# Kernel tuning notes

Measured on AMD Instinct MI355X. Metric: run time of the kernel, lower is better.

## Reference

```python
import jax, jax.numpy as jnp
import numpy as np
import math

B = 524288
D = 4
CTX = 64
HID = 128
IN_DIM = 2 + CTX  # keep_idx len is 2 for every mask
# default_masks_D(4, 10) dedups to exactly these 4 masks (torch module therefore has 4 layers)
KEEP = ((0, 1), (1, 2), (2, 3), (0, 3))
TRANS = ((2, 3), (0, 3), (0, 1), (1, 2))
L = 4


def _mlp(x, W1, b1, W2, b2, W3, b3):
    # MLP(in_dim, out_dim, hidden=128, depth=2): Lin+GELU, Lin+GELU, Lin
    x = jax.nn.gelu(x @ W1 + b1, approximate=False)
    x = jax.nn.gelu(x @ W2 + b2, approximate=False)
    return x @ W3 + b3


def setup_inputs() -> dict:
    key = jax.random.key(0)
    ks = jax.random.split(key, 16)
    theta = jax.random.normal(ks[0], (B, D), dtype=jnp.float32)
    h = jax.random.normal(ks[1], (B, CTX), dtype=jnp.float32)
    p = lambda k, shape: jax.random.normal(k, shape, dtype=jnp.float32) * 0.02
    inp = {"theta": theta, "h": h}
    # stacked per-layer weights for s_net and t_net
    for pref, off in (("s", 2), ("t", 8)):
        inp[pref + "W1"] = p(ks[off + 0], (L, IN_DIM, HID))
        inp[pref + "b1"] = p(ks[off + 1], (L, HID))
        inp[pref + "W2"] = p(ks[off + 2], (L, HID, HID))
        inp[pref + "b2"] = p(ks[off + 3], (L, HID))
        inp[pref + "W3"] = p(ks[off + 4], (L, HID, 2))
        inp[pref + "b3"] = p(ks[off + 5], (L, 2))
    return inp


def reference(theta, h, sW1, sb1, sW2, sb2, sW3, sb3, tW1, tb1, tW2, tb2, tW3, tb3):
    # ConditionalRealNVP.log_prob(theta, h)
    x = theta
    logdet = jnp.zeros(theta.shape[0], dtype=theta.dtype)
    for i in range(L):
        keep = np.array(KEEP[i])
        trans = np.array(TRANS[i])
        xp = jnp.concatenate([x[:, keep], h], axis=1)  # [B, 66]
        s = _mlp(xp, sW1[i], sb1[i], sW2[i], sb2[i], sW3[i], sb3[i])  # [B, 2]
        t = _mlp(xp, tW1[i], tb1[i], tW2[i], tb2[i], tW3[i], tb3[i])  # [B, 2]
        x = x.at[:, trans].set(x[:, trans] * jnp.exp(s) + t)
        logdet = logdet + s.sum(axis=1)
    log_pz = -0.5 * (x ** 2).sum(axis=1) - 0.5 * D * math.log(2 * math.pi)
    return log_pz + logdet
```

## Files before the change

### kernel.cpp

```cpp
#include <hip/hip_runtime.h>
#include <hip/hip_bf16.h>

typedef short short8 __attribute__((ext_vector_type(8)));
typedef float f32x4 __attribute__((ext_vector_type(4)));
typedef float f32x2 __attribute__((ext_vector_type(2)));
typedef unsigned short u16;
typedef unsigned int u32;
typedef u32 u32x4 __attribute__((ext_vector_type(4)));

#define NL_STRIDE 57344
#define OFF_W1F 0
#define OFF_W2F 16384
#define OFF_W3F 49152
#define OFF_W1K 53248
#define OFF_B1  54272
#define OFF_B2  54784
#define OFF_B3  55296

__device__ __forceinline__ u16 f2bf(float f) {
  union { float f; unsigned int u; } v; v.f = f;
  unsigned int r = v.u + 0x7fffu + ((v.u >> 16) & 1u);
  return (u16)(r >> 16);
}

__device__ __forceinline__ u32 pack_bf16_2(float a, float b) {
  union { float f; u32 u; } x, y; x.f = a; y.f = b;
  u32 ra = x.u + 0x8000u, rb = y.u + 0x8000u;
  return (ra >> 16) | (rb & 0xffff0000u);
}

__device__ __forceinline__ f32x2 gelu2(f32x2 x) {
  f32x2 u = x * x;
  f32x2 t = u * 0.00417617f + (-0.0560330f);
  t = t * u + 0.394326f;
  f32x2 s = x * t + 0.5f;
  s.x = __builtin_amdgcn_fmed3f(s.x, 0.0f, 1.0f);
  s.y = __builtin_amdgcn_fmed3f(s.y, 0.0f, 1.0f);
  return x * s;
}

__device__ __forceinline__ int kperm(int k) {
  int b = k & 31;
  return (k & ~31) | ((b >> 1) | ((b & 1) << 4));
}

__global__ __launch_bounds__(256) void prep_kernel(
    const float* __restrict__ sW1, const float* __restrict__ sb1,
    const float* __restrict__ sW2, const float* __restrict__ sb2,
    const float* __restrict__ sW3, const float* __restrict__ sb3,
    const float* __restrict__ tW1, const float* __restrict__ tb1,
    const float* __restrict__ tW2, const float* __restrict__ tb2,
    const float* __restrict__ tW3, const float* __restrict__ tb3,
    char* __restrict__ ws)
{
  int nl = blockIdx.x;
  int layer = nl >> 1, net = nl & 1;
  const float* W1 = net ? tW1 : sW1;
  const float* W2 = net ? tW2 : sW2;
  const float* W3 = net ? tW3 : sW3;
  const float* B1 = net ? tb1 : sb1;
  const float* B2 = net ? tb2 : sb2;
  const float* B3 = net ? tb3 : sb3;
  char* base = ws + (size_t)nl * NL_STRIDE;
  int e = blockIdx.y * 256 + (int)threadIdx.x;

  if (e < 8192) {
    int kt = e >> 12, rem = e & 4095, nt = rem >> 9, r2 = rem & 511;
    int l = r2 >> 3, j = r2 & 7;
    int k = kt * 32 + (l >> 4) * 8 + j, n = nt * 16 + (l & 15);
    ((u16*)(base + OFF_W1F))[e] = f2bf(W1[layer * 8448 + (2 + k) * 128 + n]);
  } else if (e < 24576) {
    int e2 = e - 8192;
    int kt = e2 >> 12, nt = (e2 >> 9) & 7, l = (e2 >> 3) & 63, j = e2 & 7;
    int k = kt * 32 + (l >> 4) * 8 + j, n = nt * 16 + (l & 15);
    ((u16*)(base + OFF_W2F))[e2] = f2bf(W2[layer * 16384 + kperm(k) * 128 + n]);
  } else if (e < 26624) {
    int e3 = e - 24576;
    int kt = e3 >> 9, l = (e3 >> 3) & 63, j = e3 & 7;
    int k = kt * 32 + (l >> 4) * 8 + j, n = l & 15;
    float v = (n < 2) ? W3[layer * 256 + kperm(k) * 2 + n] : 0.0f;
    ((u16*)(base + OFF_W3F))[e3] = f2bf(v);
  } else if (e < 26880) {
    int e4 = e - 26624; int r = e4 >> 7, n = e4 & 127;
    ((float*)(base + OFF_W1K))[e4] = W1[layer * 8448 + r * 128 + n];
  } else if (e < 27008) {
    int e5 = e - 26880; ((float*)(base + OFF_B1))[e5] = B1[layer * 128 + e5];
  } else if (e < 27136) {
    int e6 = e - 27008; ((float*)(base + OFF_B2))[e6] = B2[layer * 128 + e6];
  } else if (e < 27138) {
    int e7 = e - 27136; ((float*)(base + OFF_B3))[e7] = B3[layer * 2 + e7];
  }
}

__global__ __launch_bounds__(256, 2) void realnvp_kernel(
    const float* __restrict__ theta, const float* __restrict__ h_g,
    const char* __restrict__ ws, float* __restrict__ out)
{
  __shared__ __align__(16) u16 hs[128 * 72];
  __shared__ __align__(16) u16 hid[128 * 136];
  __shared__ float x_lds[128 * 4];
  __shared__ float sbuf[2 * 128 * 2];

  const int tid = (int)threadIdx.x;
  const int row0 = (int)blockIdx.x * 128;
  const int wv = tid >> 6, lane = tid & 63, q = lane >> 4, lr = lane & 15;

  if (tid < 128) {
    float4 t4 = *(const float4*)(theta + (size_t)(row0 + tid) * 4);
    x_lds[tid * 4 + 0] = t4.x; x_lds[tid * 4 + 1] = t4.y;
    x_lds[tid * 4 + 2] = t4.z; x_lds[tid * 4 + 3] = t4.w;
  }
  {
    int r = tid >> 1, hf = tid & 1;
    const float* src = h_g + (size_t)(row0 + r) * 64 + hf * 32;
    u16* dst = &hs[r * 72 + hf * 32];
#pragma unroll
    for (int c = 0; c < 32; c += 8) {
      float4 f0 = *(const float4*)(src + c);
      float4 f1 = *(const float4*)(src + c + 4);
      u32x4 o;
      o[0] = pack_bf16_2(f0.x, f0.y);
      o[1] = pack_bf16_2(f0.z, f0.w);
      o[2] = pack_bf16_2(f1.x, f1.y);
      o[3] = pack_bf16_2(f1.z, f1.w);
      *(u32x4*)(dst + c) = o;
    }
  }
  __syncthreads();

  float logdet = 0.0f;
  const f32x4 zero4 = {0.f, 0.f, 0.f, 0.f};
  const int col0 = wv * 32 + lr;
  u32* hidw = (u32*)&hid[wv * 32 + lr * 2];

#pragma unroll 1
  for (int layer = 0; layer < 4; ++layer) {
    int k0 = (0x0210 >> (layer * 4)) & 15;
    int k1 = (0x3321 >> (layer * 4)) & 15;

#pragma unroll 1
    for (int net = 0; net < 2; ++net) {
      const char* base = ws + (size_t)(layer * 2 + net) * NL_STRIDE;
      const u16* w1f = (const u16*)(base + OFF_W1F);
      const u16* w2f = (const u16*)(base + OFF_W2F);
      const u16* w3f = (const u16*)(base + OFF_W3F);
      const float* w1k = (const float*)(base + OFF_W1K);
      const float* b1 = (const float*)(base + OFF_B1);
      const float* b2 = (const float*)(base + OFF_B2);
      const float* b3 = (const float*)(base + OFF_B3);

      f32x4 acc[8][2];
#pragma unroll
      for (int mt = 0; mt < 8; ++mt) { acc[mt][0] = zero4; acc[mt][1] = zero4; }
      {
        const u16* abase = &hs[lr * 72 + q * 8];
#pragma unroll
        for (int kt = 0; kt < 2; ++kt) {
          short8 a[8];
#pragma unroll
          for (int mt = 0; mt < 8; ++mt)
            a[mt] = *(const short8*)(abase + mt * (16 * 72) + kt * 32);
          short8 b0 = *(const short8*)(w1f + (kt * 8 + wv * 2 + 0) * 512 + lane * 8);
          short8 b1v = *(const short8*)(w1f + (kt * 8 + wv * 2 + 1) * 512 + lane * 8);
#pragma unroll
          for (int mt = 0; mt < 8; ++mt) {
            acc[mt][0] = __builtin_amdgcn_mfma_f32_16x16x32_bf16(a[mt], b0, acc[mt][0], 0, 0, 0);
            acc[mt][1] = __builtin_amdgcn_mfma_f32_16x16x32_bf16(a[mt], b1v, acc[mt][1], 0, 0, 0);
          }
        }
      }
      f32x2 wk0 = {w1k[col0],       w1k[col0 + 16]};
      f32x2 wk1 = {w1k[128 + col0], w1k[128 + col0 + 16]};
      f32x2 bb  = {b1[col0],        b1[col0 + 16]};
      __syncthreads();
#pragma unroll
      for (int mt = 0; mt < 8; ++mt) {
        int rb = mt * 16 + q * 4;
#pragma unroll
        for (int r = 0; r < 4; ++r) {
          int row = rb + r;
          float xk0 = x_lds[row * 4 + k0], xk1 = x_lds[row * 4 + k1];
          f32x2 v = {acc[mt][0][r], acc[mt][1][r]};
          v = wk0 * xk0 + v;
          v = wk1 * xk1 + v;
          v = v + bb;
          f32x2 g = gelu2(v);
          hidw[row * 68] = pack_bf16_2(g.x, g.y);
        }
      }
      __syncthreads();

      f32x4 acc2[8][2];
#pragma unroll
      for (int mt = 0; mt < 8; ++mt) { acc2[mt][0] = zero4; acc2[mt][1] = zero4; }
      {
        const u16* hbase = &hid[lr * 136 + q * 8];
#pragma unroll
        for (int kt = 0; kt < 4; ++kt) {
          short8 a[8];
#pragma unroll
          for (int mt = 0; mt < 8; ++mt)
            a[mt] = *(const short8*)(hbase + mt * (16 * 136) + kt * 32);
          short8 b0 = *(const short8*)(w2f + (kt * 8 + wv * 2 + 0) * 512 + lane * 8);
          short8 b1v = *(const short8*)(w2f + (kt * 8 + wv * 2 + 1) * 512 + lane * 8);
#pragma unroll
          for (int mt = 0; mt < 8; ++mt) {
            acc2[mt][0] = __builtin_amdgcn_mfma_f32_16x16x32_bf16(a[mt], b0, acc2[mt][0], 0, 0, 0);
            acc2[mt][1] = __builtin_amdgcn_mfma_f32_16x16x32_bf16(a[mt], b1v, acc2[mt][1], 0, 0, 0);
          }
        }
      }
      f32x2 cb = {b2[col0], b2[col0 + 16]};
      __syncthreads();
#pragma unroll
      for (int mt = 0; mt < 8; ++mt) {
        int rb = mt * 16 + q * 4;
#pragma unroll
        for (int r = 0; r < 4; ++r) {
          int row = rb + r;
          f32x2 v = {acc2[mt][0][r], acc2[mt][1][r]};
          f32x2 g = gelu2(v + cb);
          hidw[row * 68] = pack_bf16_2(g.x, g.y);
        }
      }
      __syncthreads();

      f32x4 acc3[2]; acc3[0] = zero4; acc3[1] = zero4;
#pragma unroll
      for (int kt = 0; kt < 4; ++kt) {
        short8 b = *(const short8*)(w3f + kt * 512 + lane * 8);
#pragma unroll
        for (int i = 0; i < 2; ++i) {
          short8 a = *(const short8*)(&hid[((wv * 2 + i) * 16 + lr) * 136 + kt * 32 + q * 8]);
          acc3[i] = __builtin_amdgcn_mfma_f32_16x16x32_bf16(a, b, acc3[i], 0, 0, 0);
        }
      }
      if (lr < 2) {
        float bbs = b3[lr];
#pragma unroll
        for (int i = 0; i < 2; ++i) {
          int rb = (wv * 2 + i) * 16 + q * 4;
#pragma unroll
          for (int r = 0; r < 4; ++r)
            sbuf[net * 256 + (rb + r) * 2 + lr] = acc3[i][r] + bbs;
        }
      }
      __syncthreads();
    }

    if (tid < 128) {
      float s0 = sbuf[tid * 2 + 0], s1 = sbuf[tid * 2 + 1];
      float t0 = sbuf[256 + tid * 2 + 0], t1 = sbuf[256 + tid * 2 + 1];
      int a0 = (0x1002 >> (layer * 4)) & 15;
      int a1 = (0x2133 >> (layer * 4)) & 15;
      x_lds[tid * 4 + a0] = x_lds[tid * 4 + a0] * __expf(s0) + t0;
      x_lds[tid * 4 + a1] = x_lds[tid * 4 + a1] * __expf(s1) + t1;
      logdet += s0 + s1;
    }
    __syncthreads();
  }

  if (tid < 128) {
    float x0 = x_lds[tid * 4 + 0], x1 = x_lds[tid * 4 + 1];
    float x2 = x_lds[tid * 4 + 2], x3 = x_lds[tid * 4 + 3];
    out[row0 + tid] = -0.5f * (x0 * x0 + x1 * x1 + x2 * x2 + x3 * x3)
                      - 3.6757541328f + logdet;
  }
}

extern "C" void kernel_launch(void* const* d_in, const int* in_sizes, int n_in,
                              void* d_out, int out_size, void* d_ws, size_t ws_size,
                              hipStream_t stream) {
  (void)in_sizes; (void)n_in; (void)out_size; (void)ws_size;
  const float* theta = (const float*)d_in[0];
  const float* h     = (const float*)d_in[1];
  const float* sW1 = (const float*)d_in[2],  *sb1 = (const float*)d_in[3];
  const float* sW2 = (const float*)d_in[4],  *sb2 = (const float*)d_in[5];
  const float* sW3 = (const float*)d_in[6],  *sb3 = (const float*)d_in[7];
  const float* tW1 = (const float*)d_in[8],  *tb1 = (const float*)d_in[9];
  const float* tW2 = (const float*)d_in[10], *tb2 = (const float*)d_in[11];
  const float* tW3 = (const float*)d_in[12], *tb3 = (const float*)d_in[13];
  float* out = (float*)d_out;
  char* ws = (char*)d_ws;

  dim3 pgrid(8, 107);
  prep_kernel<<<pgrid, 256, 0, stream>>>(sW1, sb1, sW2, sb2, sW3, sb3,
                                         tW1, tb1, tW2, tb2, tW3, tb3, ws);
  realnvp_kernel<<<4096, 256, 0, stream>>>(theta, h, (const char*)ws, out);
}
```

Before: 638.6 us.

## Split GEMM work by rows per wave and keep bf16 context in registers

Each wave now owns 32 rows and computes all 128 hidden columns, instead of 32 columns across all 128 rows. The context tile is converted to bf16 once and held in registers as MFMA A-fragments, which removes the shared-memory staging buffer. Bias and first-layer key weights are permuted so they can be read as paired vectors, and the layer loop is fully unrolled with constant indices. Occupancy is raised to 4 blocks per CU. The trade-off is more global/L2 weight loads per wave (B fragments now cover all 8 column tiles) and higher register pressure under the tighter launch bound.

```diff
diff --git a/kernel.cpp b/kernel.cpp
--- a/kernel.cpp
+++ b/kernel.cpp
@@ -82,23 +82,22 @@
     ((u16*)(base + OFF_W3F))[e3] = f2bf(v);
   } else if (e < 26880) {
     int e4 = e - 26624; int r = e4 >> 7, n = e4 & 127;
-    ((float*)(base + OFF_W1K))[e4] = W1[layer * 8448 + r * 128 + n];
+    ((float*)(base + OFF_W1K))[e4] = W1[layer * 8448 + r * 128 + kperm(n)];
   } else if (e < 27008) {
-    int e5 = e - 26880; ((float*)(base + OFF_B1))[e5] = B1[layer * 128 + e5];
+    int e5 = e - 26880; ((float*)(base + OFF_B1))[e5] = B1[layer * 128 + kperm(e5)];
   } else if (e < 27136) {
-    int e6 = e - 27008; ((float*)(base + OFF_B2))[e6] = B2[layer * 128 + e6];
+    int e6 = e - 27008; ((float*)(base + OFF_B2))[e6] = B2[layer * 128 + kperm(e6)];
   } else if (e < 27138) {
     int e7 = e - 27136; ((float*)(base + OFF_B3))[e7] = B3[layer * 2 + e7];
   }
 }
 
-__global__ __launch_bounds__(256, 2) void realnvp_kernel(
+__global__ __launch_bounds__(256, 4) void realnvp_kernel(
     const float* __restrict__ theta, const float* __restrict__ h_g,
     const char* __restrict__ ws, float* __restrict__ out)
 {
-  __shared__ __align__(16) u16 hs[128 * 72];
   __shared__ __align__(16) u16 hid[128 * 136];
-  __shared__ float x_lds[128 * 4];
+  __shared__ __align__(16) float x_lds[128 * 4];
   __shared__ float sbuf[2 * 128 * 2];
 
   const int tid = (int)threadIdx.x;
@@ -110,33 +109,32 @@
     x_lds[tid * 4 + 0] = t4.x; x_lds[tid * 4 + 1] = t4.y;
     x_lds[tid * 4 + 2] = t4.z; x_lds[tid * 4 + 3] = t4.w;
   }
-  {
-    int r = tid >> 1, hf = tid & 1;
-    const float* src = h_g + (size_t)(row0 + r) * 64 + hf * 32;
-    u16* dst = &hs[r * 72 + hf * 32];
-#pragma unroll
-    for (int c = 0; c < 32; c += 8) {
-      float4 f0 = *(const float4*)(src + c);
-      float4 f1 = *(const float4*)(src + c + 4);
-      u32x4 o;
-      o[0] = pack_bf16_2(f0.x, f0.y);
-      o[1] = pack_bf16_2(f0.z, f0.w);
-      o[2] = pack_bf16_2(f1.x, f1.y);
-      o[3] = pack_bf16_2(f1.z, f1.w);
-      *(u32x4*)(dst + c) = o;
+
+  short8 hf[2][2];
+#pragma unroll
+  for (int i = 0; i < 2; ++i)
+#pragma unroll
+    for (int kt = 0; kt < 2; ++kt) {
+      const float* src = h_g + (size_t)(row0 + wv * 32 + i * 16 + lr) * 64 + kt * 32 + q * 8;
+      float4 f0 = *(const float4*)(src);
+      float4 f1 = *(const float4*)(src + 4);
+      union { u32x4 u; short8 s; } cv;
+      cv.u[0] = pack_bf16_2(f0.x, f0.y);
+      cv.u[1] = pack_bf16_2(f0.z, f0.w);
+      cv.u[2] = pack_bf16_2(f1.x, f1.y);
+      cv.u[3] = pack_bf16_2(f1.z, f1.w);
+      hf[i][kt] = cv.s;
     }
-  }
   __syncthreads();
 
   float logdet = 0.0f;
   const f32x4 zero4 = {0.f, 0.f, 0.f, 0.f};
-  const int col0 = wv * 32 + lr;
-  u32* hidw = (u32*)&hid[wv * 32 + lr * 2];
-
-#pragma unroll 1
+  constexpr int KEEP0[4] = {0, 1, 2, 0}, KEEP1[4] = {1, 2, 3, 3};
+  constexpr int TR0[4]   = {2, 0, 0, 1}, TR1[4]   = {3, 3, 1, 2};
+
+#pragma unroll
   for (int layer = 0; layer < 4; ++layer) {
-    int k0 = (0x0210 >> (layer * 4)) & 15;
-    int k1 = (0x3321 >> (layer * 4)) & 15;
+    const int k0 = KEEP0[layer], k1 = KEEP1[layer];
 
 #pragma unroll 1
     for (int net = 0; net < 2; ++net) {
@@ -149,80 +147,87 @@
       const float* b2 = (const float*)(base + OFF_B2);
       const float* b3 = (const float*)(base + OFF_B3);
 
-      f32x4 acc[8][2];
-#pragma unroll
-      for (int mt = 0; mt < 8; ++mt) { acc[mt][0] = zero4; acc[mt][1] = zero4; }
-      {
-        const u16* abase = &hs[lr * 72 + q * 8];
-#pragma unroll
-        for (int kt = 0; kt < 2; ++kt) {
-          short8 a[8];
-#pragma unroll
-          for (int mt = 0; mt < 8; ++mt)
-            a[mt] = *(const short8*)(abase + mt * (16 * 72) + kt * 32);
-          short8 b0 = *(const short8*)(w1f + (kt * 8 + wv * 2 + 0) * 512 + lane * 8);
-          short8 b1v = *(const short8*)(w1f + (kt * 8 + wv * 2 + 1) * 512 + lane * 8);
-#pragma unroll
-          for (int mt = 0; mt < 8; ++mt) {
-            acc[mt][0] = __builtin_amdgcn_mfma_f32_16x16x32_bf16(a[mt], b0, acc[mt][0], 0, 0, 0);
-            acc[mt][1] = __builtin_amdgcn_mfma_f32_16x16x32_bf16(a[mt], b1v, acc[mt][1], 0, 0, 0);
+      f32x4 acc[2][8];
+#pragma unroll
+      for (int i = 0; i < 2; ++i)
+#pragma unroll
+        for (int nt = 0; nt < 8; ++nt) acc[i][nt] = zero4;
+#pragma unroll
+      for (int kt = 0; kt < 2; ++kt)
+#pragma unroll
+        for (int a = 0; a < 4; ++a) {
+          short8 b0 = *(const short8*)(w1f + (kt * 8 + 2 * a + 0) * 512 + lane * 8);
+          short8 b1v = *(const short8*)(w1f + (kt * 8 + 2 * a + 1) * 512 + lane * 8);
+#pragma unroll
+          for (int i = 0; i < 2; ++i) {
+            acc[i][2 * a]     = __builtin_amdgcn_mfma_f32_16x16x32_bf16(hf[i][kt], b0, acc[i][2 * a], 0, 0, 0);
+            acc[i][2 * a + 1] = __builtin_amdgcn_mfma_f32_16x16x32_bf16(hf[i][kt], b1v, acc[i][2 * a + 1], 0, 0, 0);
           }
         }
-      }
-      f32x2 wk0 = {w1k[col0],       w1k[col0 + 16]};
-      f32x2 wk1 = {w1k[128 + col0], w1k[128 + col0 + 16]};
-      f32x2 bb  = {b1[col0],        b1[col0 + 16]};
-      __syncthreads();
-#pragma unroll
-      for (int mt = 0; mt < 8; ++mt) {
-        int rb = mt * 16 + q * 4;
+      f32x2 wk0v[4], wk1v[4], bbv[4];
+#pragma unroll
+      for (int a = 0; a < 4; ++a) {
+        wk0v[a] = *(const f32x2*)(w1k + a * 32 + 2 * lr);
+        wk1v[a] = *(const f32x2*)(w1k + 128 + a * 32 + 2 * lr);
+        bbv[a]  = *(const f32x2*)(b1 + a * 32 + 2 * lr);
+      }
+      __syncthreads();
+#pragma unroll
+      for (int i = 0; i < 2; ++i)
 #pragma unroll
         for (int r = 0; r < 4; ++r) {
-          int row = rb + r;
-          float xk0 = x_lds[row * 4 + k0], xk1 = x_lds[row * 4 + k1];
-          f32x2 v = {acc[mt][0][r], acc[mt][1][r]};
-          v = wk0 * xk0 + v;
-          v = wk1 * xk1 + v;
-          v = v + bb;
-          f32x2 g = gelu2(v);
-          hidw[row * 68] = pack_bf16_2(g.x, g.y);
-        }
-      }
-      __syncthreads();
-
-      f32x4 acc2[8][2];
-#pragma unroll
-      for (int mt = 0; mt < 8; ++mt) { acc2[mt][0] = zero4; acc2[mt][1] = zero4; }
-      {
-        const u16* hbase = &hid[lr * 136 + q * 8];
-#pragma unroll
-        for (int kt = 0; kt < 4; ++kt) {
-          short8 a[8];
-#pragma unroll
-          for (int mt = 0; mt < 8; ++mt)
-            a[mt] = *(const short8*)(hbase + mt * (16 * 136) + kt * 32);
-          short8 b0 = *(const short8*)(w2f + (kt * 8 + wv * 2 + 0) * 512 + lane * 8);
-          short8 b1v = *(const short8*)(w2f + (kt * 8 + wv * 2 + 1) * 512 + lane * 8);
-#pragma unroll
-          for (int mt = 0; mt < 8; ++mt) {
-            acc2[mt][0] = __builtin_amdgcn_mfma_f32_16x16x32_bf16(a[mt], b0, acc2[mt][0], 0, 0, 0);
-            acc2[mt][1] = __builtin_amdgcn_mfma_f32_16x16x32_bf16(a[mt], b1v, acc2[mt][1], 0, 0, 0);
+          int row = wv * 32 + i * 16 + q * 4 + r;
+          f32x4 xr = *(const f32x4*)(x_lds + row * 4);
+          float xk0 = xr[k0], xk1 = xr[k1];
+          u32* wrow = (u32*)&hid[row * 136];
+#pragma unroll
+          for (int a = 0; a < 4; ++a) {
+            f32x2 v = {acc[i][2 * a][r], acc[i][2 * a + 1][r]};
+            v = wk0v[a] * xk0 + v;
+            v = wk1v[a] * xk1 + v;
+            v = v + bbv[a];
+            f32x2 g = gelu2(v);
+            wrow[a * 16 + lr] = pack_bf16_2(g.x, g.y);
           }
         }
-      }
-      f32x2 cb = {b2[col0], b2[col0 + 16]};
-      __syncthreads();
-#pragma unroll
-      for (int mt = 0; mt < 8; ++mt) {
-        int rb = mt * 16 + q * 4;
+      __syncthreads();
+
+      f32x4 acc2[2][8];
+#pragma unroll
+      for (int i = 0; i < 2; ++i)
+#pragma unroll
+        for (int nt = 0; nt < 8; ++nt) acc2[i][nt] = zero4;
+#pragma unroll
+      for (int kt = 0; kt < 4; ++kt) {
+        short8 a0 = *(const short8*)(&hid[(wv * 32 + lr) * 136 + kt * 32 + q * 8]);
+        short8 a1 = *(const short8*)(&hid[(wv * 32 + 16 + lr) * 136 + kt * 32 + q * 8]);
+#pragma unroll
+        for (int a = 0; a < 4; ++a) {
+          short8 b0 = *(const short8*)(w2f + (kt * 8 + 2 * a + 0) * 512 + lane * 8);
+          short8 b1v = *(const short8*)(w2f + (kt * 8 + 2 * a + 1) * 512 + lane * 8);
+          acc2[0][2 * a]     = __builtin_amdgcn_mfma_f32_16x16x32_bf16(a0, b0, acc2[0][2 * a], 0, 0, 0);
+          acc2[1][2 * a]     = __builtin_amdgcn_mfma_f32_16x16x32_bf16(a1, b0, acc2[1][2 * a], 0, 0, 0);
+          acc2[0][2 * a + 1] = __builtin_amdgcn_mfma_f32_16x16x32_bf16(a0, b1v, acc2[0][2 * a + 1], 0, 0, 0);
+          acc2[1][2 * a + 1] = __builtin_amdgcn_mfma_f32_16x16x32_bf16(a1, b1v, acc2[1][2 * a + 1], 0, 0, 0);
+        }
+      }
+      f32x2 cbv[4];
+#pragma unroll
+      for (int a = 0; a < 4; ++a) cbv[a] = *(const f32x2*)(b2 + a * 32 + 2 * lr);
+      __syncthreads();
+#pragma unroll
+      for (int i = 0; i < 2; ++i)
 #pragma unroll
         for (int r = 0; r < 4; ++r) {
-          int row = rb + r;
-          f32x2 v = {acc2[mt][0][r], acc2[mt][1][r]};
-          f32x2 g = gelu2(v + cb);
-          hidw[row * 68] = pack_bf16_2(g.x, g.y);
-        }
-      }
+          int row = wv * 32 + i * 16 + q * 4 + r;
+          u32* wrow = (u32*)&hid[row * 136];
+#pragma unroll
+          for (int a = 0; a < 4; ++a) {
+            f32x2 v = {acc2[i][2 * a][r], acc2[i][2 * a + 1][r]};
+            f32x2 g = gelu2(v + cbv[a]);
+            wrow[a * 16 + lr] = pack_bf16_2(g.x, g.y);
+          }
+        }
       __syncthreads();
 
       f32x4 acc3[2]; acc3[0] = zero4; acc3[1] = zero4;
@@ -251,8 +256,7 @@
     if (tid < 128) {
       float s0 = sbuf[tid * 2 + 0], s1 = sbuf[tid * 2 + 1];
       float t0 = sbuf[256 + tid * 2 + 0], t1 = sbuf[256 + tid * 2 + 1];
-      int a0 = (0x1002 >> (layer * 4)) & 15;
-      int a1 = (0x2133 >> (layer * 4)) & 15;
+      const int a0 = TR0[layer], a1 = TR1[layer];
       x_lds[tid * 4 + a0] = x_lds[tid * 4 + a0] * __expf(s0) + t0;
       x_lds[tid * 4 + a1] = x_lds[tid * 4 + a1] * __expf(s1) + t1;
       logdet += s0 + s1;
```

Result: slower. 802.8 us (+25.7%).

## Split each 128-row block across 8 waves with 2D M/N wave tiling

Applied to the files above, without the earlier changes.

Raises the block from 256 to 512 threads and splits the work across waves in both directions: each wave now handles half the rows (64) and a quarter of the hidden columns. This halves per-wave accumulators and A-fragment registers, which should allow more waves in flight, and W2 B-fragments are now prefetched one k-step ahead. Hidden columns are permuted so each lane writes an adjacent bf16 pair, and the prep kernel permutes W1k, b1 and b2 to match. The cost is redundant B-fragment loads, since both row-halves fetch the same weights, plus more waves taking part in each barrier.

```diff
diff --git a/kernel.cpp b/kernel.cpp
--- a/kernel.cpp
+++ b/kernel.cpp
@@ -82,28 +82,29 @@
     ((u16*)(base + OFF_W3F))[e3] = f2bf(v);
   } else if (e < 26880) {
     int e4 = e - 26624; int r = e4 >> 7, n = e4 & 127;
-    ((float*)(base + OFF_W1K))[e4] = W1[layer * 8448 + r * 128 + n];
+    ((float*)(base + OFF_W1K))[e4] = W1[layer * 8448 + r * 128 + kperm(n)];
   } else if (e < 27008) {
-    int e5 = e - 26880; ((float*)(base + OFF_B1))[e5] = B1[layer * 128 + e5];
+    int e5 = e - 26880; ((float*)(base + OFF_B1))[e5] = B1[layer * 128 + kperm(e5)];
   } else if (e < 27136) {
-    int e6 = e - 27008; ((float*)(base + OFF_B2))[e6] = B2[layer * 128 + e6];
+    int e6 = e - 27008; ((float*)(base + OFF_B2))[e6] = B2[layer * 128 + kperm(e6)];
   } else if (e < 27138) {
     int e7 = e - 27136; ((float*)(base + OFF_B3))[e7] = B3[layer * 2 + e7];
   }
 }
 
-__global__ __launch_bounds__(256, 2) void realnvp_kernel(
+__global__ __launch_bounds__(512, 4) void realnvp_kernel(
     const float* __restrict__ theta, const float* __restrict__ h_g,
     const char* __restrict__ ws, float* __restrict__ out)
 {
   __shared__ __align__(16) u16 hs[128 * 72];
   __shared__ __align__(16) u16 hid[128 * 136];
-  __shared__ float x_lds[128 * 4];
+  __shared__ __align__(16) float x_lds[128 * 4];
   __shared__ float sbuf[2 * 128 * 2];
 
   const int tid = (int)threadIdx.x;
   const int row0 = (int)blockIdx.x * 128;
-  const int wv = tid >> 6, lane = tid & 63, q = lane >> 4, lr = lane & 15;
+  const int wave = tid >> 6, lane = tid & 63, q = lane >> 4, lr = lane & 15;
+  const int mh = wave & 1, nq = wave >> 1;
 
   if (tid < 128) {
     float4 t4 = *(const float4*)(theta + (size_t)(row0 + tid) * 4);
@@ -111,11 +112,11 @@
     x_lds[tid * 4 + 2] = t4.z; x_lds[tid * 4 + 3] = t4.w;
   }
   {
-    int r = tid >> 1, hf = tid & 1;
-    const float* src = h_g + (size_t)(row0 + r) * 64 + hf * 32;
-    u16* dst = &hs[r * 72 + hf * 32];
-#pragma unroll
-    for (int c = 0; c < 32; c += 8) {
+    int r = tid >> 2, sg = tid & 3;
+    const float* src = h_g + (size_t)(row0 + r) * 64 + sg * 16;
+    u16* dst = &hs[r * 72 + sg * 16];
+#pragma unroll
+    for (int c = 0; c < 16; c += 8) {
       float4 f0 = *(const float4*)(src + c);
       float4 f1 = *(const float4*)(src + c + 4);
       u32x4 o;
@@ -130,13 +131,11 @@
 
   float logdet = 0.0f;
   const f32x4 zero4 = {0.f, 0.f, 0.f, 0.f};
-  const int col0 = wv * 32 + lr;
-  u32* hidw = (u32*)&hid[wv * 32 + lr * 2];
 
 #pragma unroll 1
   for (int layer = 0; layer < 4; ++layer) {
-    int k0 = (0x0210 >> (layer * 4)) & 15;
-    int k1 = (0x3321 >> (layer * 4)) & 15;
+    const int k0 = (0x0210 >> (layer * 4)) & 15;
+    const int k1 = (0x3321 >> (layer * 4)) & 15;
 
 #pragma unroll 1
     for (int net = 0; net < 2; ++net) {
@@ -149,101 +148,110 @@
       const float* b2 = (const float*)(base + OFF_B2);
       const float* b3 = (const float*)(base + OFF_B3);
 
-      f32x4 acc[8][2];
-#pragma unroll
-      for (int mt = 0; mt < 8; ++mt) { acc[mt][0] = zero4; acc[mt][1] = zero4; }
+      f32x4 acc[4][2];
+#pragma unroll
+      for (int i = 0; i < 4; ++i) { acc[i][0] = zero4; acc[i][1] = zero4; }
       {
-        const u16* abase = &hs[lr * 72 + q * 8];
+        short8 b00 = *(const short8*)(w1f + (0 * 8 + 2 * nq + 0) * 512 + lane * 8);
+        short8 b01 = *(const short8*)(w1f + (0 * 8 + 2 * nq + 1) * 512 + lane * 8);
+        short8 b10 = *(const short8*)(w1f + (1 * 8 + 2 * nq + 0) * 512 + lane * 8);
+        short8 b11 = *(const short8*)(w1f + (1 * 8 + 2 * nq + 1) * 512 + lane * 8);
+        const u16* abase = &hs[(64 * mh + lr) * 72 + q * 8];
 #pragma unroll
         for (int kt = 0; kt < 2; ++kt) {
-          short8 a[8];
-#pragma unroll
-          for (int mt = 0; mt < 8; ++mt)
-            a[mt] = *(const short8*)(abase + mt * (16 * 72) + kt * 32);
-          short8 b0 = *(const short8*)(w1f + (kt * 8 + wv * 2 + 0) * 512 + lane * 8);
-          short8 b1v = *(const short8*)(w1f + (kt * 8 + wv * 2 + 1) * 512 + lane * 8);
-#pragma unroll
-          for (int mt = 0; mt < 8; ++mt) {
-            acc[mt][0] = __builtin_amdgcn_mfma_f32_16x16x32_bf16(a[mt], b0, acc[mt][0], 0, 0, 0);
-            acc[mt][1] = __builtin_amdgcn_mfma_f32_16x16x32_bf16(a[mt], b1v, acc[mt][1], 0, 0, 0);
-          }
-        }
-      }
-      f32x2 wk0 = {w1k[col0],       w1k[col0 + 16]};
-      f32x2 wk1 = {w1k[128 + col0], w1k[128 + col0 + 16]};
-      f32x2 bb  = {b1[col0],        b1[col0 + 16]};
-      __syncthreads();
-#pragma unroll
-      for (int mt = 0; mt < 8; ++mt) {
-        int rb = mt * 16 + q * 4;
+          short8 A0 = *(const short8*)(abase + 0 * (16 * 72) + kt * 32);
+          short8 A1 = *(const short8*)(abase + 1 * (16 * 72) + kt * 32);
+          short8 A2 = *(const short8*)(abase + 2 * (16 * 72) + kt * 32);
+          short8 A3 = *(const short8*)(abase + 3 * (16 * 72) + kt * 32);
+          short8 b0 = kt ? b10 : b00, b1v = kt ? b11 : b01;
+          acc[0][0] = __builtin_amdgcn_mfma_f32_16x16x32_bf16(A0, b0, acc[0][0], 0, 0, 0);
+          acc[1][0] = __builtin_amdgcn_mfma_f32_16x16x32_bf16(A1, b0, acc[1][0], 0, 0, 0);
+          acc[2][0] = __builtin_amdgcn_mfma_f32_16x16x32_bf16(A2, b0, acc[2][0], 0, 0, 0);
+          acc[3][0] = __builtin_amdgcn_mfma_f32_16x16x32_bf16(A3, b0, acc[3][0], 0, 0, 0);
+          acc[0][1] = __builtin_amdgcn_mfma_f32_16x16x32_bf16(A0, b1v, acc[0][1], 0, 0, 0);
+          acc[1][1] = __builtin_amdgcn_mfma_f32_16x16x32_bf16(A1, b1v, acc[1][1], 0, 0, 0);
+          acc[2][1] = __builtin_amdgcn_mfma_f32_16x16x32_bf16(A2, b1v, acc[2][1], 0, 0, 0);
+          acc[3][1] = __builtin_amdgcn_mfma_f32_16x16x32_bf16(A3, b1v, acc[3][1], 0, 0, 0);
+        }
+      }
+      f32x2 wk0 = *(const f32x2*)(w1k + nq * 32 + 2 * lr);
+      f32x2 wk1 = *(const f32x2*)(w1k + 128 + nq * 32 + 2 * lr);
+      f32x2 bb  = *(const f32x2*)(b1 + nq * 32 + 2 * lr);
+#pragma unroll
+      for (int i = 0; i < 4; ++i)
 #pragma unroll
         for (int r = 0; r < 4; ++r) {
-          int row = rb + r;
+          int row = 64 * mh + 16 * i + q * 4 + r;
           float xk0 = x_lds[row * 4 + k0], xk1 = x_lds[row * 4 + k1];
-          f32x2 v = {acc[mt][0][r], acc[mt][1][r]};
+          f32x2 v = {acc[i][0][r], acc[i][1][r]};
           v = wk0 * xk0 + v;
           v = wk1 * xk1 + v;
           v = v + bb;
           f32x2 g = gelu2(v);
-          hidw[row * 68] = pack_bf16_2(g.x, g.y);
-        }
-      }
-      __syncthreads();
-
-      f32x4 acc2[8][2];
-#pragma unroll
-      for (int mt = 0; mt < 8; ++mt) { acc2[mt][0] = zero4; acc2[mt][1] = zero4; }
+          ((u32*)&hid[row * 136])[nq * 16 + lr] = pack_bf16_2(g.x, g.y);
+        }
+      __syncthreads();
+
+      f32x4 acc2[4][2];
+#pragma unroll
+      for (int i = 0; i < 4; ++i) { acc2[i][0] = zero4; acc2[i][1] = zero4; }
       {
-        const u16* hbase = &hid[lr * 136 + q * 8];
+        const u16* hbase = &hid[(64 * mh + lr) * 136 + q * 8];
+        short8 nb0 = *(const short8*)(w2f + (0 * 8 + 2 * nq + 0) * 512 + lane * 8);
+        short8 nb1 = *(const short8*)(w2f + (0 * 8 + 2 * nq + 1) * 512 + lane * 8);
+        short8 pb0 = *(const short8*)(w2f + (1 * 8 + 2 * nq + 0) * 512 + lane * 8);
+        short8 pb1 = *(const short8*)(w2f + (1 * 8 + 2 * nq + 1) * 512 + lane * 8);
 #pragma unroll
         for (int kt = 0; kt < 4; ++kt) {
-          short8 a[8];
-#pragma unroll
-          for (int mt = 0; mt < 8; ++mt)
-            a[mt] = *(const short8*)(hbase + mt * (16 * 136) + kt * 32);
-          short8 b0 = *(const short8*)(w2f + (kt * 8 + wv * 2 + 0) * 512 + lane * 8);
-          short8 b1v = *(const short8*)(w2f + (kt * 8 + wv * 2 + 1) * 512 + lane * 8);
-#pragma unroll
-          for (int mt = 0; mt < 8; ++mt) {
-            acc2[mt][0] = __builtin_amdgcn_mfma_f32_16x16x32_bf16(a[mt], b0, acc2[mt][0], 0, 0, 0);
-            acc2[mt][1] = __builtin_amdgcn_mfma_f32_16x16x32_bf16(a[mt], b1v, acc2[mt][1], 0, 0, 0);
+          short8 b0 = nb0, b1v = nb1;
+          nb0 = pb0; nb1 = pb1;
+          if (kt < 2) {
+            pb0 = *(const short8*)(w2f + ((kt + 2) * 8 + 2 * nq + 0) * 512 + lane * 8);
+            pb1 = *(const short8*)(w2f + ((kt + 2) * 8 + 2 * nq + 1) * 512 + lane * 8);
           }
-        }
-      }
-      f32x2 cb = {b2[col0], b2[col0 + 16]};
-      __syncthreads();
-#pragma unroll
-      for (int mt = 0; mt < 8; ++mt) {
-        int rb = mt * 16 + q * 4;
+          short8 A0 = *(const short8*)(hbase + 0 * (16 * 136) + kt * 32);
+          short8 A1 = *(const short8*)(hbase + 1 * (16 * 136) + kt * 32);
+          short8 A2 = *(const short8*)(hbase + 2 * (16 * 136) + kt * 32);
+          short8 A3 = *(const short8*)(hbase + 3 * (16 * 136) + kt * 32);
+          acc2[0][0] = __builtin_amdgcn_mfma_f32_16x16x32_bf16(A0, b0, acc2[0][0], 0, 0, 0);
+          acc2[1][0] = __builtin_amdgcn_mfma_f32_16x16x32_bf16(A1, b0, acc2[1][0], 0, 0, 0);
+          acc2[2][0] = __builtin_amdgcn_mfma_f32_16x16x32_bf16(A2, b0, acc2[2][0], 0, 0, 0);
+          acc2[3][0] = __builtin_amdgcn_mfma_f32_16x16x32_bf16(A3, b0, acc2[3][0], 0, 0, 0);
+          acc2[0][1] = __builtin_amdgcn_mfma_f32_16x16x32_bf16(A0, b1v, acc2[0][1], 0, 0, 0);
+          acc2[1][1] = __builtin_amdgcn_mfma_f32_16x16x32_bf16(A1, b1v, acc2[1][1], 0, 0, 0);
+          acc2[2][1] = __builtin_amdgcn_mfma_f32_16x16x32_bf16(A2, b1v, acc2[2][1], 0, 0, 0);
+          acc2[3][1] = __builtin_amdgcn_mfma_f32_16x16x32_bf16(A3, b1v, acc2[3][1], 0, 0, 0);
+        }
+      }
+      f32x2 cb = *(const f32x2*)(b2 + nq * 32 + 2 * lr);
+      __syncthreads();
+#pragma unroll
+      for (int i = 0; i < 4; ++i)
 #pragma unroll
         for (int r = 0; r < 4; ++r) {
-          int row = rb + r;
-          f32x2 v = {acc2[mt][0][r], acc2[mt][1][r]};
+          int row = 64 * mh + 16 * i + q * 4 + r;
+          f32x2 v = {acc2[i][0][r], acc2[i][1][r]};
           f32x2 g = gelu2(v + cb);
-          hidw[row * 68] = pack_bf16_2(g.x, g.y);
-        }
-      }
-      __syncthreads();
-
-      f32x4 acc3[2]; acc3[0] = zero4; acc3[1] = zero4;
-#pragma unroll
-      for (int kt = 0; kt < 4; ++kt) {
-        short8 b = *(const short8*)(w3f + kt * 512 + lane * 8);
-#pragma unroll
-        for (int i = 0; i < 2; ++i) {
-          short8 a = *(const short8*)(&hid[((wv * 2 + i) * 16 + lr) * 136 + kt * 32 + q * 8]);
-          acc3[i] = __builtin_amdgcn_mfma_f32_16x16x32_bf16(a, b, acc3[i], 0, 0, 0);
+          ((u32*)&hid[row * 136])[nq * 16 + lr] = pack_bf16_2(g.x, g.y);
+        }
+      __syncthreads();
+
+      f32x4 acc3 = zero4;
+      {
+        const u16* hbase3 = &hid[(16 * wave + lr) * 136 + q * 8];
+#pragma unroll
+        for (int kt = 0; kt < 4; ++kt) {
+          short8 b = *(const short8*)(w3f + kt * 512 + lane * 8);
+          short8 a = *(const short8*)(hbase3 + kt * 32);
+          acc3 = __builtin_amdgcn_mfma_f32_16x16x32_bf16(a, b, acc3, 0, 0, 0);
         }
       }
       if (lr < 2) {
         float bbs = b3[lr];
-#pragma unroll
-        for (int i = 0; i < 2; ++i) {
-          int rb = (wv * 2 + i) * 16 + q * 4;
-#pragma unroll
-          for (int r = 0; r < 4; ++r)
-            sbuf[net * 256 + (rb + r) * 2 + lr] = acc3[i][r] + bbs;
-        }
+        int rb = 16 * wave + q * 4;
+#pragma unroll
+        for (int r = 0; r < 4; ++r)
+          sbuf[net * 256 + (rb + r) * 2 + lr] = acc3[r] + bbs;
       }
       __syncthreads();
     }
@@ -251,8 +259,8 @@
     if (tid < 128) {
       float s0 = sbuf[tid * 2 + 0], s1 = sbuf[tid * 2 + 1];
       float t0 = sbuf[256 + tid * 2 + 0], t1 = sbuf[256 + tid * 2 + 1];
-      int a0 = (0x1002 >> (layer * 4)) & 15;
-      int a1 = (0x2133 >> (layer * 4)) & 15;
+      const int a0 = (0x1002 >> (layer * 4)) & 15;
+      const int a1 = (0x2133 >> (layer * 4)) & 15;
       x_lds[tid * 4 + a0] = x_lds[tid * 4 + a0] * __expf(s0) + t0;
       x_lds[tid * 4 + a1] = x_lds[tid * 4 + a1] * __expf(s1) + t1;
       logdet += s0 + s1;
@@ -286,5 +294,5 @@
   dim3 pgrid(8, 107);
   prep_kernel<<<pgrid, 256, 0, stream>>>(sW1, sb1, sW2, sb2, sW3, sb3,
                                          tW1, tb1, tW2, tb2, tW3, tb3, ws);
-  realnvp_kernel<<<4096, 256, 0, stream>>>(theta, h, (const char*)ws, out);
-}
+  realnvp_kernel<<<4096, 512, 0, stream>>>(theta, h, (const char*)ws, out);
+}
```

After: 617.7 us. 1.03x faster.
